# Performance work log

Hardware: AMD Instinct MI355X
Metric: run time of the kernel (lower is better)

## Reference

```python
import jax, jax.numpy as jnp
import numpy as np

N = 768           # atoms
C = 128           # channels (layer_dims = [128]*4)
A = 8             # atom types
RBF = 4
RBF_LOW, RBF_HIGH = 0.0, 2.5
EPS = 1e-12

# Levi-Civita tensor for the 1x1->1 tensor product
_E = np.zeros((3, 3, 3), np.float32)
_E[0, 1, 2] = _E[1, 2, 0] = _E[2, 0, 1] = 1.0
_E[0, 2, 1] = _E[2, 1, 0] = _E[1, 0, 2] = -1.0
EIJK = jnp.asarray(_E)


def setup_inputs() -> dict:
    key = jax.random.key(0)
    ks = jax.random.split(key, 16)
    r = jax.random.normal(ks[0], (N, 3), jnp.float32) * 2.0
    one_hot = jax.nn.one_hot(jax.random.randint(ks[1], (N,), 0, A), A, dtype=jnp.float32)

    def W(k, shape, fan_in):
        return jax.random.normal(k, shape, jnp.float32) / np.sqrt(fan_in).astype(np.float32)

    return dict(
        r=r, one_hot=one_hot,
        embed_W=W(ks[2], (C, A), A), embed_b=jnp.zeros((C,), jnp.float32),
        # 12 radial nets: layer0 uses ids 0-1, layer1 ids 2-6, layer2 ids 7-11
        Rw1=W(ks[3], (12, RBF, C), RBF), Rb1=jnp.zeros((12, C), jnp.float32),
        Rw2=W(ks[4], (12, C, C), C), Rb2=jnp.zeros((12, C), jnp.float32),
        si0_w0=W(ks[5], (C, C), C), si0_b0=jnp.zeros((C,), jnp.float32),
        si0_w1=W(ks[6], (C, C), C),
        si1_w0=W(ks[7], (C, 2 * C), 2 * C), si1_b0=jnp.zeros((C,), jnp.float32),
        si1_w1=W(ks[8], (C, 3 * C), 3 * C),
        si2_w0=W(ks[9], (C, 2 * C), 2 * C), si2_b0=jnp.zeros((C,), jnp.float32),
        si2_w1=W(ks[10], (C, 3 * C), 3 * C),
        nl_b0=jnp.zeros((C,), jnp.float32), nl_b1=jnp.zeros((C,), jnp.float32),
        pred_W=W(ks[11], (A, C), C), pred_b=jnp.zeros((A,), jnp.float32),
    )


def _gated(x, b):
    # norm-gated equivariant nonlinearity for l=1 features [N, C, 3]
    n = jnp.sqrt(jnp.maximum(jnp.sum(x * x, -1), EPS))
    return x * (jax.nn.elu(b[None, :] + n) / n)[..., None]


def reference(r, one_hot, embed_W, embed_b, Rw1, Rb1, Rw2, Rb2,
              si0_w0, si0_b0, si0_w1, si1_w0, si1_b0, si1_w1,
              si2_w0, si2_b0, si2_w1, nl_b0, nl_b1, pred_W, pred_b):
    rij = r[:, None, :] - r[None, :, :]                     # [N,N,3]
    dij = jnp.sqrt(jnp.maximum(jnp.sum(rij * rij, -1), EPS))  # [N,N]
    u = rij / (dij[..., None] + 1e-8)                        # unit vectors
    centers = jnp.linspace(RBF_LOW, RBF_HIGH, RBF)
    gamma = RBF / (RBF_HIGH - RBF_LOW)                       # 1 / spacing
    rbf = jnp.exp(-gamma * jnp.square(dij[..., None] - centers))  # [N,N,RBF]

    def radial(i):  # per-filter radial net on rbf features -> [N,N,C]
        h = jax.nn.relu(jnp.einsum('abr,rc->abc', rbf, Rw1[i]) + Rb1[i])
        return jnp.einsum('abc,cd->abd', h, Rw2[i]) + Rb2[i]

    def si(x, w, b=None):  # self-interaction linear over channel dim f
        y = jnp.einsum('afm,gf->agm', x, w)
        return y if b is None else y + b[:, None]

    e = (one_hot @ embed_W.T + embed_b)[..., None]           # [N,C,1]

    # layer 0: only an l=0 input exists
    c00 = jnp.einsum('abf,bfm->afm', radial(0), e)                 # 0x0->0
    c01 = jnp.einsum('abf,abi,bf->afi', radial(1), u, e[..., 0])   # 0x1->1
    x0 = jax.nn.elu(si(c00, si0_w0, si0_b0))
    x1 = _gated(si(c01, si0_w1), nl_b0)

    def full_layer(x0, x1, ri, w0, b0, w1):
        a0 = jnp.einsum('abf,bfm->afm', radial(ri), x0)                        # 0x0->0
        b1 = jnp.einsum('abf,abi,bf->afi', radial(ri + 1), u, x0[..., 0])      # 0x1->1
        a1 = jnp.einsum('abf,bfm->afm', radial(ri + 2), x1)                    # 1x0->1
        o0 = jnp.einsum('abf,abj,bfj->af', radial(ri + 3), u, x1)[..., None]   # 1x1->0
        o1 = jnp.einsum('ijk,abf,abj,bfk->afi', EIJK, radial(ri + 4), u, x1)   # 1x1->1
        y0 = si(jnp.concatenate([a0, o0], 1), w0, b0)   # [N,2C,1] -> [N,C,1]
        y1 = si(jnp.concatenate([b1, a1, o1], 1), w1)   # [N,3C,3] -> [N,C,3]
        return y0, y1

    x0, x1 = full_layer(x0, x1, 2, si1_w0, si1_b0, si1_w1)
    x0, x1 = jax.nn.elu(x0), _gated(x1, nl_b1)
    x0, x1 = full_layer(x0, x1, 7, si2_w0, si2_b0, si2_w1)  # last layer: no nonlinearity

    atom = (x0[..., 0] @ pred_W.T + pred_b)[..., None]      # [N,A,1]
    # (probability_scalars, missing_coordinates, atom_type_scalars)
    return x0, x1, atom
```

## Files before the change

kernel.cpp:

```cpp
#include <hip/hip_runtime.h>
#include <hip/hip_fp16.h>
#include <math.h>


constexpr int   N_     = 768;
constexpr int   C_     = 128;
constexpr int   M_     = 512;
constexpr int   NSPLIT = 3;
constexpr int   NB_    = N_ / NSPLIT;
constexpr int   TA_    = 3;
constexpr float DMAX_  = 6.4f;
constexpr float GAMMA_ = 1.6f;

__device__ inline float lerp_vd(float fr, __half2 vd) {
    return fmaf(fr, __half2float(__high2half(vd)), __half2float(__low2half(vd)));
}

__global__ __launch_bounds__(256) void build_table_kernel(
    const float* __restrict__ Rw1, const float* __restrict__ Rb1,
    const float* __restrict__ Rw2, const float* __restrict__ Rb2,
    __half2* __restrict__ tab, float delta)
{
    const int f  = threadIdx.x & 127, fh = threadIdx.x >> 7;
    const int m0 = blockIdx.x * 4;

    __shared__ float hs[2][5][C_];

    float rbf[5][4];
    const float cent[4] = {0.0f, 2.5f / 3.0f, 5.0f / 3.0f, 2.5f};
#pragma unroll
    for (int mm = 0; mm < 5; ++mm) {
        int m = m0 + mm; if (m > M_ - 1) m = M_ - 1;
        const float d = (float)m * delta;
#pragma unroll
        for (int k = 0; k < 4; ++k) {
            const float t = d - cent[k];
            rbf[mm][k] = expf(-GAMMA_ * t * t);
        }
    }

    for (int ii = 0; ii < 6; ++ii) {
        const int i = fh * 6 + ii;
        float w1v[4];
#pragma unroll
        for (int k = 0; k < 4; ++k) w1v[k] = Rw1[(i * 4 + k) * C_ + f];
        const float b1v = Rb1[i * C_ + f];

        __syncthreads();
#pragma unroll
        for (int mm = 0; mm < 5; ++mm) {
            float acc = b1v;
#pragma unroll
            for (int k = 0; k < 4; ++k) acc = fmaf(rbf[mm][k], w1v[k], acc);
            hs[fh][mm][f] = fmaxf(acc, 0.0f);
        }
        __syncthreads();

        const float b2v = Rb2[i * C_ + f];
        float out[5] = {b2v, b2v, b2v, b2v, b2v};
        for (int c = 0; c < C_; ++c) {
            const float w = Rw2[(i * C_ + c) * C_ + f];
#pragma unroll
            for (int mm = 0; mm < 5; ++mm) out[mm] = fmaf(hs[fh][mm][c], w, out[mm]);
        }
#pragma unroll
        for (int mm = 0; mm < 4; ++mm) {
            const int m = m0 + mm;
            if (m < M_)
                tab[((size_t)m * 12 + i) * C_ + f] =
                    __floats2half2_rn(out[mm], out[mm + 1] - out[mm]);
        }
    }
}

__global__ __launch_bounds__(256) void embed_kernel(
    const float* __restrict__ onehot, const float* __restrict__ eW,
    const float* __restrict__ eb, float* __restrict__ e)
{
    const int idx = blockIdx.x * 256 + threadIdx.x;
    const int b = idx >> 7, f = idx & 127;
    float acc = eb[f];
#pragma unroll
    for (int t = 0; t < 8; ++t) acc = fmaf(onehot[b * 8 + t], eW[f * 8 + t], acc);
    e[idx] = acc;
}

__device__ inline void pair_setup(const float* __restrict__ r, int a, int bbase,
                                  int tid, int RI, float4* pair, int* qoff)
{
    const float rax = r[a * 3 + 0], ray = r[a * 3 + 1], raz = r[a * 3 + 2];
    for (int i = tid; i < NB_; i += 256) {
        const int b = bbase + i;
        const float dx = rax - r[b * 3 + 0];
        const float dy = ray - r[b * 3 + 1];
        const float dz = raz - r[b * 3 + 2];
        const float d2 = fmaf(dx, dx, fmaf(dy, dy, dz * dz));
        const float d  = sqrtf(fmaxf(d2, 1e-12f));
        const float inv = 1.0f / (d + 1e-8f);
        const float t = d * ((float)(M_ - 1) / DMAX_);
        int q = (int)t; q = q > M_ - 2 ? M_ - 2 : q;
        const float fr = fminf(t - (float)q, 1.0f);
        pair[i] = make_float4(dx * inv, dy * inv, dz * inv, fr);
        qoff[i] = (q * 12 + RI) * C_;
    }
}

__global__ __launch_bounds__(256, 8) void pair0_kernel(
    const float* __restrict__ r, const float* __restrict__ e,
    const __half2* __restrict__ tab, float* __restrict__ P)
{
    const int a = blockIdx.x / NSPLIT, p = blockIdx.x - a * NSPLIT;
    const int tid = threadIdx.x;
    const int f = tid & 127, part = tid >> 7;
    const int bbase = p * NB_;

    __shared__ float4 pair[NB_];
    __shared__ int    qoff[NB_];
    __shared__ float  sred[4][2][C_];

    pair_setup(r, a, bbase, tid, 0, pair, qoff);
    __syncthreads();

    float c00 = 0.f, cx = 0.f, cy = 0.f, cz = 0.f;
    const __half2* tabf = tab + f;
    const float*   ef   = e + (size_t)bbase * C_ + f;
    const int iBeg = part * (NB_ / 2), iEnd = iBeg + (NB_ / 2);
    for (int i = iBeg; i < iEnd; ++i) {
        const float4 pr = pair[i];
        const __half2* tp = tabf + qoff[i];
        const __half2 h0 = tp[0], h1 = tp[C_];
        const float eb_ = ef[(size_t)i * C_];
        const float fr = pr.w;
        const float t0 = lerp_vd(fr, h0);
        const float t1 = lerp_vd(fr, h1);
        c00 = fmaf(t0, eb_, c00);
        const float te = t1 * eb_;
        cx = fmaf(te, pr.x, cx); cy = fmaf(te, pr.y, cy); cz = fmaf(te, pr.z, cz);
    }

    sred[0][part][f] = c00;
    sred[1][part][f] = cx;
    sred[2][part][f] = cy;
    sred[3][part][f] = cz;
    __syncthreads();

    for (int idx = tid; idx < 4 * C_; idx += 256) {
        const int k = idx >> 7, c = idx & 127;
        P[((size_t)(p * N_ + a) * 4) * C_ + idx] = sred[k][0][c] + sred[k][1][c];
    }
}

__global__ __launch_bounds__(256, 8) void pairF_kernel(
    const float* __restrict__ r, const uint2* __restrict__ xin,
    const __half2* __restrict__ tab, int RI, float* __restrict__ P)
{
    const int a = blockIdx.x / NSPLIT, p = blockIdx.x - a * NSPLIT;
    const int tid = threadIdx.x;
    const int f = tid & 127, part = tid >> 7;
    const int bbase = p * NB_;

    __shared__ float4 pair[NB_];
    __shared__ int    qoff[NB_];
    __shared__ float  sred[11][2][C_];

    pair_setup(r, a, bbase, tid, RI, pair, qoff);
    __syncthreads();

    float a0 = 0.f, b1x = 0.f, b1y = 0.f, b1z = 0.f;
    float a1x = 0.f, a1y = 0.f, a1z = 0.f;
    float o0 = 0.f, o1x = 0.f, o1y = 0.f, o1z = 0.f;

    const __half2* tabf = tab + f;
    const uint2*   xf   = xin + (size_t)bbase * C_ + f;
    const int iBeg = part * (NB_ / 2), iEnd = iBeg + (NB_ / 2);
    for (int i = iBeg; i < iEnd; ++i) {
        const float4 pr = pair[i];
        const __half2* tp = tabf + qoff[i];
        const __half2 h0 = tp[0 * C_], h1 = tp[1 * C_], h2 = tp[2 * C_];
        const __half2 h3 = tp[3 * C_], h4 = tp[4 * C_];
        const uint2 xw = xf[(size_t)i * C_];

        const float fr = pr.w;
        const float t0 = lerp_vd(fr, h0);
        const float t1 = lerp_vd(fr, h1);
        const float t2 = lerp_vd(fr, h2);
        const float t3 = lerp_vd(fr, h3);
        const float t4 = lerp_vd(fr, h4);

        const __half2 xh01 = *(const __half2*)&xw.x;
        const __half2 xh23 = *(const __half2*)&xw.y;
        const float x0b = __half2float(__low2half(xh01));
        const float xbx = __half2float(__high2half(xh01));
        const float xby = __half2float(__low2half(xh23));
        const float xbz = __half2float(__high2half(xh23));

        a0 = fmaf(t0, x0b, a0);
        const float tb = t1 * x0b;
        b1x = fmaf(tb, pr.x, b1x); b1y = fmaf(tb, pr.y, b1y); b1z = fmaf(tb, pr.z, b1z);
        a1x = fmaf(t2, xbx, a1x); a1y = fmaf(t2, xby, a1y); a1z = fmaf(t2, xbz, a1z);
        const float ud = fmaf(pr.x, xbx, fmaf(pr.y, xby, pr.z * xbz));
        o0 = fmaf(t3, ud, o0);
        const float crx = pr.y * xbz - pr.z * xby;
        const float cry = pr.z * xbx - pr.x * xbz;
        const float crz = pr.x * xby - pr.y * xbx;
        o1x = fmaf(t4, crx, o1x); o1y = fmaf(t4, cry, o1y); o1z = fmaf(t4, crz, o1z);
    }

    sred[0][part][f] = a0;
    sred[1][part][f] = b1x; sred[2][part][f] = b1y; sred[3][part][f] = b1z;
    sred[4][part][f] = a1x; sred[5][part][f] = a1y; sred[6][part][f] = a1z;
    sred[7][part][f] = o0;
    sred[8][part][f] = o1x; sred[9][part][f] = o1y; sred[10][part][f] = o1z;
    __syncthreads();

    for (int idx = tid; idx < 11 * C_; idx += 256) {
        const int k = idx >> 7, c = idx & 127;
        P[((size_t)(p * N_ + a) * 11) * C_ + idx] = sred[k][0][c] + sred[k][1][c];
    }
}

__global__ __launch_bounds__(512) void finish0_kernel(
    const float* __restrict__ P,
    const float* __restrict__ w0, const float* __restrict__ b0v,
    const float* __restrict__ w1, const float* __restrict__ nlb,
    uint2* __restrict__ xout)
{
    const int a0_ = blockIdx.x * TA_, tid = threadIdx.x;
    const int f = tid & 127, j = tid >> 7;

    __shared__ float s[TA_][4 * C_];
    __shared__ float ys[TA_][4 * C_];

    for (int t = 0; t < TA_; ++t)
        for (int idx = tid; idx < 4 * C_; idx += 512) {
            float acc = 0.f;
            for (int sp = 0; sp < NSPLIT; ++sp)
                acc += P[((size_t)(sp * N_ + a0_ + t) * 4) * C_ + idx];
            s[t][idx] = acc;
        }
    __syncthreads();

    float acc[TA_];
    if (j == 0) {
        const float b0 = b0v[f];
#pragma unroll
        for (int t = 0; t < TA_; ++t) acc[t] = b0;
        const float4* w = (const float4*)(w0 + (size_t)f * C_);
        for (int c4 = 0; c4 < C_ / 4; ++c4) {
            const float4 wv = w[c4];
#pragma unroll
            for (int t = 0; t < TA_; ++t) {
                const float4 sv = *(const float4*)&s[t][c4 * 4];
                acc[t] = fmaf(wv.x, sv.x, acc[t]);
                acc[t] = fmaf(wv.y, sv.y, acc[t]);
                acc[t] = fmaf(wv.z, sv.z, acc[t]);
                acc[t] = fmaf(wv.w, sv.w, acc[t]);
            }
        }
    } else {
#pragma unroll
        for (int t = 0; t < TA_; ++t) acc[t] = 0.f;
        const float4* w = (const float4*)(w1 + (size_t)f * C_);
        for (int c4 = 0; c4 < C_ / 4; ++c4) {
            const float4 wv = w[c4];
#pragma unroll
            for (int t = 0; t < TA_; ++t) {
                const float4 sv = *(const float4*)&s[t][j * C_ + c4 * 4];
                acc[t] = fmaf(wv.x, sv.x, acc[t]);
                acc[t] = fmaf(wv.y, sv.y, acc[t]);
                acc[t] = fmaf(wv.z, sv.z, acc[t]);
                acc[t] = fmaf(wv.w, sv.w, acc[t]);
            }
        }
    }
#pragma unroll
    for (int t = 0; t < TA_; ++t) ys[t][j * C_ + f] = acc[t];
    __syncthreads();

    if (tid < TA_ * C_) {
        const int t = tid >> 7, ff = tid & 127;
        const float y0 = ys[t][ff];
        const float yx = ys[t][C_ + ff], yy = ys[t][2 * C_ + ff], yz = ys[t][3 * C_ + ff];
        const float x0v = y0 > 0.f ? y0 : expm1f(y0);
        const float nsq = fmaf(yx, yx, fmaf(yy, yy, yz * yz));
        const float nn  = sqrtf(fmaxf(nsq, 1e-12f));
        const float g   = nlb[ff] + nn;
        const float sc  = (g > 0.f ? g : expm1f(g)) / nn;
        uint2 w;
        *(__half2*)&w.x = __floats2half2_rn(x0v, yx * sc);
        *(__half2*)&w.y = __floats2half2_rn(yy * sc, yz * sc);
        xout[(size_t)(a0_ + t) * C_ + ff] = w;
    }
}

template <bool NONLIN, bool LAST>
__global__ __launch_bounds__(512) void finishF_kernel(
    const float* __restrict__ P,
    const float* __restrict__ w0, const float* __restrict__ b0v,
    const float* __restrict__ w1, const float* __restrict__ nlb,
    uint2* __restrict__ xout,
    float* __restrict__ out, const float* __restrict__ predW,
    const float* __restrict__ predb)
{
    const int a0_ = blockIdx.x * TA_, tid = threadIdx.x;
    const int f = tid & 127, j = tid >> 7;

    __shared__ float s[TA_][11 * C_];
    __shared__ float ys[TA_][4 * C_];

    for (int t = 0; t < TA_; ++t)
        for (int idx = tid; idx < 11 * C_; idx += 512) {
            float acc = 0.f;
            for (int sp = 0; sp < NSPLIT; ++sp)
                acc += P[((size_t)(sp * N_ + a0_ + t) * 11) * C_ + idx];
            s[t][idx] = acc;
        }
    __syncthreads();

    float acc[TA_];
    if (j == 0) {
        const float b0 = b0v[f];
#pragma unroll
        for (int t = 0; t < TA_; ++t) acc[t] = b0;
        const float4* w = (const float4*)(w0 + (size_t)f * (2 * C_));
        for (int c4 = 0; c4 < C_ / 4; ++c4) {
            const float4 wa = w[c4];
            const float4 wb = w[C_ / 4 + c4];
#pragma unroll
            for (int t = 0; t < TA_; ++t) {
                const float4 s0 = *(const float4*)&s[t][c4 * 4];
                const float4 s7 = *(const float4*)&s[t][7 * C_ + c4 * 4];
                acc[t] = fmaf(wa.x, s0.x, acc[t]);
                acc[t] = fmaf(wa.y, s0.y, acc[t]);
                acc[t] = fmaf(wa.z, s0.z, acc[t]);
                acc[t] = fmaf(wa.w, s0.w, acc[t]);
                acc[t] = fmaf(wb.x, s7.x, acc[t]);
                acc[t] = fmaf(wb.y, s7.y, acc[t]);
                acc[t] = fmaf(wb.z, s7.z, acc[t]);
                acc[t] = fmaf(wb.w, s7.w, acc[t]);
            }
        }
    } else {
#pragma unroll
        for (int t = 0; t < TA_; ++t) acc[t] = 0.f;
        const float4* w = (const float4*)(w1 + (size_t)f * (3 * C_));
        for (int c4 = 0; c4 < C_ / 4; ++c4) {
            const float4 wb = w[c4];
            const float4 wa = w[C_ / 4 + c4];
            const float4 wo = w[2 * (C_ / 4) + c4];
#pragma unroll
            for (int t = 0; t < TA_; ++t) {
                const float4 sb = *(const float4*)&s[t][j * C_ + c4 * 4];
                const float4 sa = *(const float4*)&s[t][(3 + j) * C_ + c4 * 4];
                const float4 so = *(const float4*)&s[t][(7 + j) * C_ + c4 * 4];
                acc[t] = fmaf(wb.x, sb.x, acc[t]);
                acc[t] = fmaf(wb.y, sb.y, acc[t]);
                acc[t] = fmaf(wb.z, sb.z, acc[t]);
                acc[t] = fmaf(wb.w, sb.w, acc[t]);
                acc[t] = fmaf(wa.x, sa.x, acc[t]);
                acc[t] = fmaf(wa.y, sa.y, acc[t]);
                acc[t] = fmaf(wa.z, sa.z, acc[t]);
                acc[t] = fmaf(wa.w, sa.w, acc[t]);
                acc[t] = fmaf(wo.x, so.x, acc[t]);
                acc[t] = fmaf(wo.y, so.y, acc[t]);
                acc[t] = fmaf(wo.z, so.z, acc[t]);
                acc[t] = fmaf(wo.w, so.w, acc[t]);
            }
        }
    }
#pragma unroll
    for (int t = 0; t < TA_; ++t) ys[t][j * C_ + f] = acc[t];
    __syncthreads();

    if (NONLIN) {
        if (tid < TA_ * C_) {
            const int t = tid >> 7, ff = tid & 127;
            const float y0 = ys[t][ff];
            const float yx = ys[t][C_ + ff], yy = ys[t][2 * C_ + ff], yz = ys[t][3 * C_ + ff];
            const float x0v = y0 > 0.f ? y0 : expm1f(y0);
            const float nsq = fmaf(yx, yx, fmaf(yy, yy, yz * yz));
            const float nn  = sqrtf(fmaxf(nsq, 1e-12f));
            const float g   = nlb[ff] + nn;
            const float sc  = (g > 0.f ? g : expm1f(g)) / nn;
            uint2 w;
            *(__half2*)&w.x = __floats2half2_rn(x0v, yx * sc);
            *(__half2*)&w.y = __floats2half2_rn(yy * sc, yz * sc);
            xout[(size_t)(a0_ + t) * C_ + ff] = w;
        }
    }
    if (LAST) {
        if (tid < TA_ * C_) {
            const int t = tid >> 7, ff = tid & 127;
            const int a = a0_ + t;
            const float y0 = ys[t][ff];
            const float yx = ys[t][C_ + ff], yy = ys[t][2 * C_ + ff], yz = ys[t][3 * C_ + ff];
            out[a * C_ + ff] = y0;
            float* o1 = out + N_ * C_;
            o1[a * (C_ * 3) + ff * 3 + 0] = yx;
            o1[a * (C_ * 3) + ff * 3 + 1] = yy;
            o1[a * (C_ * 3) + ff * 3 + 2] = yz;
        }
        if (tid < TA_ * 8) {
            const int t = tid >> 3, o = tid & 7;
            float acc2 = predb[o];
            for (int c = 0; c < C_; ++c)
                acc2 = fmaf(predW[o * C_ + c], ys[t][c], acc2);
            out[N_ * C_ + N_ * C_ * 3 + (a0_ + t) * 8 + o] = acc2;
        }
    }
}

extern "C" void kernel_launch(void* const* d_in, const int* in_sizes, int n_in,
                              void* d_out, int out_size, void* d_ws, size_t ws_size,
                              hipStream_t stream)
{
    const float* r       = (const float*)d_in[0];
    const float* onehot  = (const float*)d_in[1];
    const float* embed_W = (const float*)d_in[2];
    const float* embed_b = (const float*)d_in[3];
    const float* Rw1     = (const float*)d_in[4];
    const float* Rb1     = (const float*)d_in[5];
    const float* Rw2     = (const float*)d_in[6];
    const float* Rb2     = (const float*)d_in[7];
    const float* si0_w0  = (const float*)d_in[8];
    const float* si0_b0  = (const float*)d_in[9];
    const float* si0_w1  = (const float*)d_in[10];
    const float* si1_w0  = (const float*)d_in[11];
    const float* si1_b0  = (const float*)d_in[12];
    const float* si1_w1  = (const float*)d_in[13];
    const float* si2_w0  = (const float*)d_in[14];
    const float* si2_b0  = (const float*)d_in[15];
    const float* si2_w1  = (const float*)d_in[16];
    const float* nl_b0   = (const float*)d_in[17];
    const float* nl_b1   = (const float*)d_in[18];
    const float* pred_W  = (const float*)d_in[19];
    const float* pred_b  = (const float*)d_in[20];
    (void)in_sizes; (void)n_in; (void)out_size; (void)ws_size;

    const float delta = DMAX_ / (float)(M_ - 1);

    char* wsb = (char*)d_ws;
    size_t off = 0;
    __half2* table = (__half2*)(wsb + off); off += (size_t)M_ * 12 * C_ * 4;
    float*   e     = (float*)(wsb + off);   off += (size_t)N_ * C_ * 4;
    uint2*   xa    = (uint2*)(wsb + off);   off += (size_t)N_ * C_ * 8;
    uint2*   xb    = (uint2*)(wsb + off);   off += (size_t)N_ * C_ * 8;
    float*   P     = (float*)(wsb + off);

    float* out = (float*)d_out;

    build_table_kernel<<<M_ / 4, 256, 0, stream>>>(Rw1, Rb1, Rw2, Rb2, table, delta);
    embed_kernel<<<(N_ * C_) / 256, 256, 0, stream>>>(onehot, embed_W, embed_b, e);

    pair0_kernel<<<NSPLIT * N_, 256, 0, stream>>>(r, e, table, P);
    finish0_kernel<<<N_ / TA_, 512, 0, stream>>>(P, si0_w0, si0_b0, si0_w1,
                                                 nl_b0, xa);
    pairF_kernel<<<NSPLIT * N_, 256, 0, stream>>>(r, xa, table, 2, P);
    finishF_kernel<true, false><<<N_ / TA_, 512, 0, stream>>>(
        P, si1_w0, si1_b0, si1_w1, nl_b1, xb, nullptr, nullptr, nullptr);

    pairF_kernel<<<NSPLIT * N_, 256, 0, stream>>>(r, xb, table, 7, P);
    finishF_kernel<false, true><<<N_ / TA_, 512, 0, stream>>>(
        P, si2_w0, si2_b0, si2_w1, nullptr, nullptr, out, pred_W, pred_b);
}
```

Baseline: 496.5 us.

## Process channel pairs per thread with packed-FP32 math and planar FP32 features

Each thread now handles two adjacent channels using 2-wide float vectors and packed half2 FMA for the table interpolation. The radial table is repacked so that one uint2 holds the values and deltas of two channels. Node features are stored as planar FP32 (scalar, x, y, z) instead of packed half, and the b-range is split across four thread groups rather than two. Launch bounds for pairF drop to 5 waves. The aim is fewer instructions per pair through packed FP32 ops, at the cost of more feature memory traffic and lower interpolation precision from the half FMA.

```diff
diff --git a/kernel.cpp b/kernel.cpp
--- a/kernel.cpp
+++ b/kernel.cpp
@@ -3,8 +3,11 @@
 #include <math.h>
 
 
+typedef float v2f __attribute__((ext_vector_type(2)));
+
 constexpr int   N_     = 768;
 constexpr int   C_     = 128;
+constexpr int   FP_    = C_ / 2;
 constexpr int   M_     = 512;
 constexpr int   NSPLIT = 3;
 constexpr int   NB_    = N_ / NSPLIT;
@@ -12,19 +15,23 @@
 constexpr float DMAX_  = 6.4f;
 constexpr float GAMMA_ = 1.6f;
 
-__device__ inline float lerp_vd(float fr, __half2 vd) {
-    return fmaf(fr, __half2float(__high2half(vd)), __half2float(__low2half(vd)));
+__device__ inline v2f vfma(v2f a, v2f b, v2f c) { return __builtin_elementwise_fma(a, b, c); }
+__device__ inline v2f sp(float x) { return (v2f){x, x}; }
+__device__ inline __half2 H2(unsigned u) { __half2 h; *(unsigned*)&h = u; return h; }
+__device__ inline v2f h2v(__half2 h) {
+    return (v2f){__half2float(__low2half(h)), __half2float(__high2half(h))};
 }
 
 __global__ __launch_bounds__(256) void build_table_kernel(
     const float* __restrict__ Rw1, const float* __restrict__ Rb1,
     const float* __restrict__ Rw2, const float* __restrict__ Rb2,
-    __half2* __restrict__ tab, float delta)
-{
-    const int f  = threadIdx.x & 127, fh = threadIdx.x >> 7;
+    uint2* __restrict__ tab, float delta)
+{
+    const int fp = threadIdx.x & 63, g = threadIdx.x >> 6;
+    const int c0 = fp * 2;
     const int m0 = blockIdx.x * 4;
 
-    __shared__ float hs[2][5][C_];
+    __shared__ float hs[4][5][C_];
 
     float rbf[5][4];
     const float cent[4] = {0.0f, 2.5f / 3.0f, 5.0f / 3.0f, 2.5f};
@@ -39,36 +46,43 @@
         }
     }
 
-    for (int ii = 0; ii < 6; ++ii) {
-        const int i = fh * 6 + ii;
-        float w1v[4];
-#pragma unroll
-        for (int k = 0; k < 4; ++k) w1v[k] = Rw1[(i * 4 + k) * C_ + f];
-        const float b1v = Rb1[i * C_ + f];
+    for (int ii = 0; ii < 3; ++ii) {
+        const int i = g * 3 + ii;
+        v2f w1v[4];
+#pragma unroll
+        for (int k = 0; k < 4; ++k)
+            w1v[k] = *(const v2f*)&Rw1[(i * 4 + k) * C_ + c0];
+        const v2f b1v = *(const v2f*)&Rb1[i * C_ + c0];
 
         __syncthreads();
 #pragma unroll
         for (int mm = 0; mm < 5; ++mm) {
-            float acc = b1v;
-#pragma unroll
-            for (int k = 0; k < 4; ++k) acc = fmaf(rbf[mm][k], w1v[k], acc);
-            hs[fh][mm][f] = fmaxf(acc, 0.0f);
+            v2f acc = b1v;
+#pragma unroll
+            for (int k = 0; k < 4; ++k) acc = vfma(sp(rbf[mm][k]), w1v[k], acc);
+            acc.x = fmaxf(acc.x, 0.0f);
+            acc.y = fmaxf(acc.y, 0.0f);
+            *(v2f*)&hs[g][mm][c0] = acc;
         }
         __syncthreads();
 
-        const float b2v = Rb2[i * C_ + f];
-        float out[5] = {b2v, b2v, b2v, b2v, b2v};
+        const v2f b2v = *(const v2f*)&Rb2[i * C_ + c0];
+        v2f out[5] = {b2v, b2v, b2v, b2v, b2v};
         for (int c = 0; c < C_; ++c) {
-            const float w = Rw2[(i * C_ + c) * C_ + f];
-#pragma unroll
-            for (int mm = 0; mm < 5; ++mm) out[mm] = fmaf(hs[fh][mm][c], w, out[mm]);
+            const v2f w = *(const v2f*)&Rw2[((size_t)i * C_ + c) * C_ + c0];
+#pragma unroll
+            for (int mm = 0; mm < 5; ++mm) out[mm] = vfma(sp(hs[g][mm][c]), w, out[mm]);
         }
 #pragma unroll
         for (int mm = 0; mm < 4; ++mm) {
             const int m = m0 + mm;
-            if (m < M_)
-                tab[((size_t)m * 12 + i) * C_ + f] =
-                    __floats2half2_rn(out[mm], out[mm + 1] - out[mm]);
+            if (m < M_) {
+                const v2f dl = out[mm + 1] - out[mm];
+                const __half2 vh = __floats2half2_rn(out[mm].x, out[mm].y);
+                const __half2 dh = __floats2half2_rn(dl.x, dl.y);
+                tab[((size_t)m * 12 + i) * FP_ + fp] =
+                    make_uint2(*(const unsigned*)&vh, *(const unsigned*)&dh);
+            }
         }
     }
 }
@@ -101,121 +115,132 @@
         int q = (int)t; q = q > M_ - 2 ? M_ - 2 : q;
         const float fr = fminf(t - (float)q, 1.0f);
         pair[i] = make_float4(dx * inv, dy * inv, dz * inv, fr);
-        qoff[i] = (q * 12 + RI) * C_;
+        qoff[i] = (q * 12 + RI) * FP_;
     }
 }
 
 __global__ __launch_bounds__(256, 8) void pair0_kernel(
     const float* __restrict__ r, const float* __restrict__ e,
-    const __half2* __restrict__ tab, float* __restrict__ P)
+    const uint2* __restrict__ tab, float* __restrict__ P)
 {
     const int a = blockIdx.x / NSPLIT, p = blockIdx.x - a * NSPLIT;
     const int tid = threadIdx.x;
-    const int f = tid & 127, part = tid >> 7;
+    const int fp = tid & 63, part = tid >> 6;
     const int bbase = p * NB_;
 
     __shared__ float4 pair[NB_];
     __shared__ int    qoff[NB_];
-    __shared__ float  sred[4][2][C_];
+    __shared__ float  sred[4][4][C_];
 
     pair_setup(r, a, bbase, tid, 0, pair, qoff);
     __syncthreads();
 
-    float c00 = 0.f, cx = 0.f, cy = 0.f, cz = 0.f;
-    const __half2* tabf = tab + f;
-    const float*   ef   = e + (size_t)bbase * C_ + f;
-    const int iBeg = part * (NB_ / 2), iEnd = iBeg + (NB_ / 2);
+    v2f c00 = sp(0.f), cx = sp(0.f), cy = sp(0.f), cz = sp(0.f);
+    const uint2* tb = tab + fp;
+    const float* ef = e + (size_t)bbase * C_ + 2 * fp;
+    const int iBeg = part * (NB_ / 4), iEnd = iBeg + (NB_ / 4);
+#pragma unroll 2
     for (int i = iBeg; i < iEnd; ++i) {
         const float4 pr = pair[i];
-        const __half2* tp = tabf + qoff[i];
-        const __half2 h0 = tp[0], h1 = tp[C_];
-        const float eb_ = ef[(size_t)i * C_];
-        const float fr = pr.w;
-        const float t0 = lerp_vd(fr, h0);
-        const float t1 = lerp_vd(fr, h1);
-        c00 = fmaf(t0, eb_, c00);
-        const float te = t1 * eb_;
-        cx = fmaf(te, pr.x, cx); cy = fmaf(te, pr.y, cy); cz = fmaf(te, pr.z, cz);
-    }
-
-    sred[0][part][f] = c00;
-    sred[1][part][f] = cx;
-    sred[2][part][f] = cy;
-    sred[3][part][f] = cz;
+        const uint2* tp = tb + qoff[i];
+        const uint2 w0 = tp[0 * FP_], w1 = tp[1 * FP_];
+        const v2f e2 = *(const v2f*)&ef[(size_t)i * C_];
+        const __half2 fr2 = __float2half2_rn(pr.w);
+        const v2f t0 = h2v(__hfma2(fr2, H2(w0.y), H2(w0.x)));
+        const v2f t1 = h2v(__hfma2(fr2, H2(w1.y), H2(w1.x)));
+        c00 = vfma(t0, e2, c00);
+        const v2f te = t1 * e2;
+        cx = vfma(te, sp(pr.x), cx);
+        cy = vfma(te, sp(pr.y), cy);
+        cz = vfma(te, sp(pr.z), cz);
+    }
+
+    *(v2f*)&sred[0][part][2 * fp] = c00;
+    *(v2f*)&sred[1][part][2 * fp] = cx;
+    *(v2f*)&sred[2][part][2 * fp] = cy;
+    *(v2f*)&sred[3][part][2 * fp] = cz;
     __syncthreads();
 
     for (int idx = tid; idx < 4 * C_; idx += 256) {
         const int k = idx >> 7, c = idx & 127;
-        P[((size_t)(p * N_ + a) * 4) * C_ + idx] = sred[k][0][c] + sred[k][1][c];
-    }
-}
-
-__global__ __launch_bounds__(256, 8) void pairF_kernel(
-    const float* __restrict__ r, const uint2* __restrict__ xin,
-    const __half2* __restrict__ tab, int RI, float* __restrict__ P)
+        P[((size_t)(p * N_ + a) * 4) * C_ + idx] =
+            sred[k][0][c] + sred[k][1][c] + sred[k][2][c] + sred[k][3][c];
+    }
+}
+
+__global__ __launch_bounds__(256, 5) void pairF_kernel(
+    const float* __restrict__ r, const float* __restrict__ xin,
+    const uint2* __restrict__ tab, int RI, float* __restrict__ P)
 {
     const int a = blockIdx.x / NSPLIT, p = blockIdx.x - a * NSPLIT;
     const int tid = threadIdx.x;
-    const int f = tid & 127, part = tid >> 7;
+    const int fp = tid & 63, part = tid >> 6;
     const int bbase = p * NB_;
 
     __shared__ float4 pair[NB_];
     __shared__ int    qoff[NB_];
-    __shared__ float  sred[11][2][C_];
+    __shared__ float  sred[11][4][C_];
 
     pair_setup(r, a, bbase, tid, RI, pair, qoff);
     __syncthreads();
 
-    float a0 = 0.f, b1x = 0.f, b1y = 0.f, b1z = 0.f;
-    float a1x = 0.f, a1y = 0.f, a1z = 0.f;
-    float o0 = 0.f, o1x = 0.f, o1y = 0.f, o1z = 0.f;
-
-    const __half2* tabf = tab + f;
-    const uint2*   xf   = xin + (size_t)bbase * C_ + f;
-    const int iBeg = part * (NB_ / 2), iEnd = iBeg + (NB_ / 2);
+    v2f a0 = sp(0.f), b1x = sp(0.f), b1y = sp(0.f), b1z = sp(0.f);
+    v2f a1x = sp(0.f), a1y = sp(0.f), a1z = sp(0.f);
+    v2f o0 = sp(0.f), o1x = sp(0.f), o1y = sp(0.f), o1z = sp(0.f);
+
+    const uint2* tb = tab + fp;
+    const float* xf = xin + ((size_t)bbase * 4) * C_ + 2 * fp;
+    const int iBeg = part * (NB_ / 4), iEnd = iBeg + (NB_ / 4);
+#pragma unroll 2
     for (int i = iBeg; i < iEnd; ++i) {
         const float4 pr = pair[i];
-        const __half2* tp = tabf + qoff[i];
-        const __half2 h0 = tp[0 * C_], h1 = tp[1 * C_], h2 = tp[2 * C_];
-        const __half2 h3 = tp[3 * C_], h4 = tp[4 * C_];
-        const uint2 xw = xf[(size_t)i * C_];
-
-        const float fr = pr.w;
-        const float t0 = lerp_vd(fr, h0);
-        const float t1 = lerp_vd(fr, h1);
-        const float t2 = lerp_vd(fr, h2);
-        const float t3 = lerp_vd(fr, h3);
-        const float t4 = lerp_vd(fr, h4);
-
-        const __half2 xh01 = *(const __half2*)&xw.x;
-        const __half2 xh23 = *(const __half2*)&xw.y;
-        const float x0b = __half2float(__low2half(xh01));
-        const float xbx = __half2float(__high2half(xh01));
-        const float xby = __half2float(__low2half(xh23));
-        const float xbz = __half2float(__high2half(xh23));
-
-        a0 = fmaf(t0, x0b, a0);
-        const float tb = t1 * x0b;
-        b1x = fmaf(tb, pr.x, b1x); b1y = fmaf(tb, pr.y, b1y); b1z = fmaf(tb, pr.z, b1z);
-        a1x = fmaf(t2, xbx, a1x); a1y = fmaf(t2, xby, a1y); a1z = fmaf(t2, xbz, a1z);
-        const float ud = fmaf(pr.x, xbx, fmaf(pr.y, xby, pr.z * xbz));
-        o0 = fmaf(t3, ud, o0);
-        const float crx = pr.y * xbz - pr.z * xby;
-        const float cry = pr.z * xbx - pr.x * xbz;
-        const float crz = pr.x * xby - pr.y * xbx;
-        o1x = fmaf(t4, crx, o1x); o1y = fmaf(t4, cry, o1y); o1z = fmaf(t4, crz, o1z);
-    }
-
-    sred[0][part][f] = a0;
-    sred[1][part][f] = b1x; sred[2][part][f] = b1y; sred[3][part][f] = b1z;
-    sred[4][part][f] = a1x; sred[5][part][f] = a1y; sred[6][part][f] = a1z;
-    sred[7][part][f] = o0;
-    sred[8][part][f] = o1x; sred[9][part][f] = o1y; sred[10][part][f] = o1z;
+        const uint2* tp = tb + qoff[i];
+        const uint2 w0 = tp[0 * FP_], w1 = tp[1 * FP_], w2 = tp[2 * FP_];
+        const uint2 w3 = tp[3 * FP_], w4 = tp[4 * FP_];
+        const float* xi = xf + (size_t)i * (4 * C_);
+        const v2f x0b = *(const v2f*)&xi[0 * C_];
+        const v2f xbx = *(const v2f*)&xi[1 * C_];
+        const v2f xby = *(const v2f*)&xi[2 * C_];
+        const v2f xbz = *(const v2f*)&xi[3 * C_];
+
+        const __half2 fr2 = __float2half2_rn(pr.w);
+        const v2f t0 = h2v(__hfma2(fr2, H2(w0.y), H2(w0.x)));
+        const v2f t1 = h2v(__hfma2(fr2, H2(w1.y), H2(w1.x)));
+        const v2f t2 = h2v(__hfma2(fr2, H2(w2.y), H2(w2.x)));
+        const v2f t3 = h2v(__hfma2(fr2, H2(w3.y), H2(w3.x)));
+        const v2f t4 = h2v(__hfma2(fr2, H2(w4.y), H2(w4.x)));
+
+        const v2f ux = sp(pr.x), uy = sp(pr.y), uz = sp(pr.z);
+
+        a0 = vfma(t0, x0b, a0);
+        const v2f te = t1 * x0b;
+        b1x = vfma(te, ux, b1x); b1y = vfma(te, uy, b1y); b1z = vfma(te, uz, b1z);
+        a1x = vfma(t2, xbx, a1x); a1y = vfma(t2, xby, a1y); a1z = vfma(t2, xbz, a1z);
+        v2f ud = xbx * ux; ud = vfma(xby, uy, ud); ud = vfma(xbz, uz, ud);
+        o0 = vfma(t3, ud, o0);
+        const v2f crx = xbz * uy - xby * uz;
+        const v2f cry = xbx * uz - xbz * ux;
+        const v2f crz = xby * ux - xbx * uy;
+        o1x = vfma(t4, crx, o1x); o1y = vfma(t4, cry, o1y); o1z = vfma(t4, crz, o1z);
+    }
+
+    *(v2f*)&sred[0][part][2 * fp]  = a0;
+    *(v2f*)&sred[1][part][2 * fp]  = b1x;
+    *(v2f*)&sred[2][part][2 * fp]  = b1y;
+    *(v2f*)&sred[3][part][2 * fp]  = b1z;
+    *(v2f*)&sred[4][part][2 * fp]  = a1x;
+    *(v2f*)&sred[5][part][2 * fp]  = a1y;
+    *(v2f*)&sred[6][part][2 * fp]  = a1z;
+    *(v2f*)&sred[7][part][2 * fp]  = o0;
+    *(v2f*)&sred[8][part][2 * fp]  = o1x;
+    *(v2f*)&sred[9][part][2 * fp]  = o1y;
+    *(v2f*)&sred[10][part][2 * fp] = o1z;
     __syncthreads();
 
     for (int idx = tid; idx < 11 * C_; idx += 256) {
         const int k = idx >> 7, c = idx & 127;
-        P[((size_t)(p * N_ + a) * 11) * C_ + idx] = sred[k][0][c] + sred[k][1][c];
+        P[((size_t)(p * N_ + a) * 11) * C_ + idx] =
+            sred[k][0][c] + sred[k][1][c] + sred[k][2][c] + sred[k][3][c];
     }
 }
 
@@ -223,7 +248,7 @@
     const float* __restrict__ P,
     const float* __restrict__ w0, const float* __restrict__ b0v,
     const float* __restrict__ w1, const float* __restrict__ nlb,
-    uint2* __restrict__ xout)
+    float* __restrict__ xout)
 {
     const int a0_ = blockIdx.x * TA_, tid = threadIdx.x;
     const int f = tid & 127, j = tid >> 7;
@@ -234,8 +259,8 @@
     for (int t = 0; t < TA_; ++t)
         for (int idx = tid; idx < 4 * C_; idx += 512) {
             float acc = 0.f;
-            for (int sp = 0; sp < NSPLIT; ++sp)
-                acc += P[((size_t)(sp * N_ + a0_ + t) * 4) * C_ + idx];
+            for (int sp_ = 0; sp_ < NSPLIT; ++sp_)
+                acc += P[((size_t)(sp_ * N_ + a0_ + t) * 4) * C_ + idx];
             s[t][idx] = acc;
         }
     __syncthreads();
@@ -286,10 +311,11 @@
         const float nn  = sqrtf(fmaxf(nsq, 1e-12f));
         const float g   = nlb[ff] + nn;
         const float sc  = (g > 0.f ? g : expm1f(g)) / nn;
-        uint2 w;
-        *(__half2*)&w.x = __floats2half2_rn(x0v, yx * sc);
-        *(__half2*)&w.y = __floats2half2_rn(yy * sc, yz * sc);
-        xout[(size_t)(a0_ + t) * C_ + ff] = w;
+        float* xo = xout + (size_t)(a0_ + t) * 4 * C_ + ff;
+        xo[0 * C_] = x0v;
+        xo[1 * C_] = yx * sc;
+        xo[2 * C_] = yy * sc;
+        xo[3 * C_] = yz * sc;
     }
 }
 
@@ -298,7 +324,7 @@
     const float* __restrict__ P,
     const float* __restrict__ w0, const float* __restrict__ b0v,
     const float* __restrict__ w1, const float* __restrict__ nlb,
-    uint2* __restrict__ xout,
+    float* __restrict__ xout,
     float* __restrict__ out, const float* __restrict__ predW,
     const float* __restrict__ predb)
 {
@@ -311,8 +337,8 @@
     for (int t = 0; t < TA_; ++t)
         for (int idx = tid; idx < 11 * C_; idx += 512) {
             float acc = 0.f;
-            for (int sp = 0; sp < NSPLIT; ++sp)
-                acc += P[((size_t)(sp * N_ + a0_ + t) * 11) * C_ + idx];
+            for (int sp_ = 0; sp_ < NSPLIT; ++sp_)
+                acc += P[((size_t)(sp_ * N_ + a0_ + t) * 11) * C_ + idx];
             s[t][idx] = acc;
         }
     __syncthreads();
@@ -382,10 +408,11 @@
             const float nn  = sqrtf(fmaxf(nsq, 1e-12f));
             const float g   = nlb[ff] + nn;
             const float sc  = (g > 0.f ? g : expm1f(g)) / nn;
-            uint2 w;
-            *(__half2*)&w.x = __floats2half2_rn(x0v, yx * sc);
-            *(__half2*)&w.y = __floats2half2_rn(yy * sc, yz * sc);
-            xout[(size_t)(a0_ + t) * C_ + ff] = w;
+            float* xo = xout + (size_t)(a0_ + t) * 4 * C_ + ff;
+            xo[0 * C_] = x0v;
+            xo[1 * C_] = yx * sc;
+            xo[2 * C_] = yy * sc;
+            xo[3 * C_] = yz * sc;
         }
     }
     if (LAST) {
@@ -441,11 +468,11 @@
 
     char* wsb = (char*)d_ws;
     size_t off = 0;
-    __half2* table = (__half2*)(wsb + off); off += (size_t)M_ * 12 * C_ * 4;
-    float*   e     = (float*)(wsb + off);   off += (size_t)N_ * C_ * 4;
-    uint2*   xa    = (uint2*)(wsb + off);   off += (size_t)N_ * C_ * 8;
-    uint2*   xb    = (uint2*)(wsb + off);   off += (size_t)N_ * C_ * 8;
-    float*   P     = (float*)(wsb + off);
+    uint2* table = (uint2*)(wsb + off); off += (size_t)M_ * 12 * FP_ * 8;
+    float* e     = (float*)(wsb + off); off += (size_t)N_ * C_ * 4;
+    float* xa    = (float*)(wsb + off); off += (size_t)N_ * 4 * C_ * 4;
+    float* xb    = (float*)(wsb + off); off += (size_t)N_ * 4 * C_ * 4;
+    float* P     = (float*)(wsb + off);
 
     float* out = (float*)d_out;
 
```

After: 556.8 us. +12.1%, slower.
